# Performance work log

Measured on AMD Instinct MI355X. Metric: run time of the kernel, lower is better.

## Reference

```python
import jax, jax.numpy as jnp
import numpy as np


def setup_inputs() -> dict:
    key = jax.random.key(0)
    k1, k2, k3, k4 = jax.random.split(key, 4)
    B, T, S, D = 256, 16, 32, 768
    return {
        "video_global": jax.random.normal(k1, (B, D), dtype=jnp.float32),
        "text_global": jax.random.normal(k2, (B, D), dtype=jnp.float32),
        "video_local": jax.random.normal(k3, (B, T, D), dtype=jnp.float32),
        "text_local": jax.random.normal(k4, (B, S, D), dtype=jnp.float32),
        "temp": jnp.zeros((1,), dtype=jnp.float32),  # log(1.0)
    }


def reference(video_global, text_global, video_local, text_local, temp):
    B = video_global.shape[0]
    logit_scale = jnp.exp(temp)[0]

    # ---- global contrastive loss ----
    global_sim = logit_scale * (video_global @ text_global.T)  # [B, B]
    diag = jnp.arange(B)
    loss_v2t = -jax.nn.log_softmax(global_sim, axis=1)[diag, diag].mean()
    loss_t2v = -jax.nn.log_softmax(global_sim, axis=0)[diag, diag].mean()
    loss_global = 0.5 * (loss_v2t + loss_t2v)

    # ---- local positive scores ----
    # paired (diagonal) local similarity: [B, T, S]
    sim_pos = logit_scale * jnp.einsum("btd,bsd->bts", video_local, text_local)
    time_weights = jax.nn.softmax(sim_pos.max(axis=-1), axis=-1)  # [B, T]
    pos_scores = (sim_pos.mean(axis=-1) * time_weights).sum(axis=1)  # [B]

    # ---- local negative scores (batched pairwise contraction) ----
    # [B, B, T, S]: video i vs text j, replacing the B*(B-1) tiny einsum loop
    sim_all = logit_scale * jnp.einsum("btd,csd->bcts", video_local, text_local)
    neg_full = (time_weights[:, None, :] * sim_all.mean(axis=-1)).sum(axis=-1)  # [B, B]

    # drop diagonal (i == j), preserving row-major loop order
    rows, cols = np.nonzero(~np.eye(B, dtype=bool))
    neg_scores = neg_full[rows, cols].reshape(B, B - 1)

    logits = jnp.concatenate([pos_scores[:, None], neg_scores], axis=-1)  # [B, B]
    loss_local = -jax.nn.log_softmax(logits, axis=-1)[:, 0].mean()

    return 0.6 * loss_global + 0.4 * loss_local
```

## Files before the change

### kernel.cpp

```cpp
#include <hip/hip_runtime.h>
#include <cmath>

#define BB 256
#define TT 16
#define SS 32
#define DD 768
#define LROW 260

__global__ __launch_bounds__(512) void hl_stage1(
    const float* __restrict__ vl, const float* __restrict__ tl,
    const float* __restrict__ temp,
    float* __restrict__ vw_ws, float* __restrict__ tb_ws)
{
    __shared__ float smem[12480];
    __shared__ float simb[512];
    __shared__ float rmax[16];
    __shared__ float twb[16];

    const int i   = blockIdx.x;
    const int tid = threadIdx.x;
    const float lsc = expf(temp[0]);

    const int slice = tid & 15;
    const int g     = tid >> 4;
    const int tg    = g >> 3;
    const int sg    = g & 7;

    const float* vli = vl + (size_t)i * TT * DD;
    const float* tli = tl + (size_t)i * SS * DD;

    float acc[4][4];
#pragma unroll
    for (int a = 0; a < 4; ++a)
#pragma unroll
        for (int b = 0; b < 4; ++b) acc[a][b] = 0.f;

    for (int c = 0; c < 3; ++c) {
        const int d0 = c << 8;
#pragma unroll
        for (int k = 0; k < 2; ++k) {
            int f4 = tid + (k << 9);
            int r  = f4 >> 6;
            int dc = (f4 & 63) << 2;
            *(float4*)&smem[r * LROW + dc] = *(const float4*)&vli[r * DD + d0 + dc];
        }
#pragma unroll
        for (int k = 0; k < 4; ++k) {
            int f4 = tid + (k << 9);
            int r  = f4 >> 6;
            int dc = (f4 & 63) << 2;
            *(float4*)&smem[(16 + r) * LROW + dc] = *(const float4*)&tli[r * DD + d0 + dc];
        }
        __syncthreads();
#pragma unroll
        for (int step = 0; step < 4; ++step) {
            const int db = (slice << 4) + (step << 2);
            float4 av[4], bv[4];
#pragma unroll
            for (int ti = 0; ti < 4; ++ti)
                av[ti] = *(const float4*)&smem[(tg * 4 + ti) * LROW + db];
#pragma unroll
            for (int sj = 0; sj < 4; ++sj)
                bv[sj] = *(const float4*)&smem[(16 + sg * 4 + sj) * LROW + db];
#pragma unroll
            for (int ti = 0; ti < 4; ++ti)
#pragma unroll
                for (int sj = 0; sj < 4; ++sj)
                    acc[ti][sj] += av[ti].x * bv[sj].x + av[ti].y * bv[sj].y
                                 + av[ti].z * bv[sj].z + av[ti].w * bv[sj].w;
        }
        __syncthreads();
    }

#pragma unroll
    for (int ti = 0; ti < 4; ++ti)
#pragma unroll
        for (int sj = 0; sj < 4; ++sj) {
            int t = tg * 4 + ti, s = sg * 4 + sj;
            smem[(t * 32 + s) * 17 + slice] = acc[ti][sj];
        }
    __syncthreads();
    {
        float ssum = 0.f;
#pragma unroll
        for (int k = 0; k < 16; ++k) ssum += smem[tid * 17 + k];
        simb[tid] = lsc * ssum;
    }
    __syncthreads();
    if (tid < 16) {
        float m = -3.0e38f;
        for (int s = 0; s < 32; ++s)
            m = fmaxf(m, simb[tid * 32 + ((s + tid) & 31)]);
        rmax[tid] = m;
    }
    __syncthreads();
    if (tid == 0) {
        float M = -3.0e38f;
        for (int t = 0; t < 16; ++t) M = fmaxf(M, rmax[t]);
        float ssum = 0.f;
        for (int t = 0; t < 16; ++t) {
            float e = expf(rmax[t] - M);
            twb[t] = e;
            ssum += e;
        }
        float inv = 1.0f / ssum;
        for (int t = 0; t < 16; ++t) twb[t] *= inv;
    }
    __syncthreads();

    for (int d = tid; d < DD; d += 512) {
        float vwv = 0.f;
#pragma unroll
        for (int t = 0; t < 16; ++t) vwv += twb[t] * vli[t * DD + d];
        vw_ws[(size_t)i * DD + d] = vwv;
        float tbv = 0.f;
#pragma unroll
        for (int s = 0; s < 32; ++s) tbv += tli[s * DD + d];
        tb_ws[(size_t)i * DD + d] = tbv * (1.0f / 32.0f);
    }
}

__global__ __launch_bounds__(256) void hl_gemm(
    const float* __restrict__ vg, const float* __restrict__ tg,
    const float* __restrict__ vw, const float* __restrict__ tb,
    const float* __restrict__ temp, float* __restrict__ cparts)
{
    __shared__ float As[16][68];
    __shared__ float Bs[16][68];
    __shared__ float Tb[64][68];

    const int b   = blockIdx.x;
    const int p   = b & 7;
    const int tj  = (b >> 3) & 3;
    const int ti  = (b >> 5) & 3;
    const int mat = b >> 7;
    const int tid = threadIdx.x;
    const float lsc = expf(temp[0]);

    const float* A  = mat ? vw : vg;
    const float* Bm = mat ? tb : tg;
    const int i0 = ti * 64, j0 = tj * 64, kb0 = p * 96;

    const int srow = tid >> 2, skq = tid & 3;
    const int tr = tid >> 4, tc = tid & 15;

    float acc[4][4];
#pragma unroll
    for (int r = 0; r < 4; ++r)
#pragma unroll
        for (int cc = 0; cc < 4; ++cc) acc[r][cc] = 0.f;

    for (int ch = 0; ch < 6; ++ch) {
        const int kb = kb0 + ch * 16;
        float4 a4 = *(const float4*)&A [(size_t)(i0 + srow) * DD + kb + skq * 4];
        float4 b4 = *(const float4*)&Bm[(size_t)(j0 + srow) * DD + kb + skq * 4];
        __syncthreads();
        As[skq * 4 + 0][srow] = a4.x; As[skq * 4 + 1][srow] = a4.y;
        As[skq * 4 + 2][srow] = a4.z; As[skq * 4 + 3][srow] = a4.w;
        Bs[skq * 4 + 0][srow] = b4.x; Bs[skq * 4 + 1][srow] = b4.y;
        Bs[skq * 4 + 2][srow] = b4.z; Bs[skq * 4 + 3][srow] = b4.w;
        __syncthreads();
#pragma unroll
        for (int k = 0; k < 16; ++k) {
            float4 av = *(const float4*)&As[k][tr * 4];
            float4 bv = *(const float4*)&Bs[k][tc * 4];
            float ar[4] = {av.x, av.y, av.z, av.w};
            float br[4] = {bv.x, bv.y, bv.z, bv.w};
#pragma unroll
            for (int r = 0; r < 4; ++r)
#pragma unroll
                for (int cc = 0; cc < 4; ++cc)
                    acc[r][cc] += ar[r] * br[cc];
        }
    }

    const int cm = mat ? 0 : 1;
    float* Cp = cparts + ((size_t)p * 3 + cm) * 65536;
#pragma unroll
    for (int r = 0; r < 4; ++r) {
        float4 v = {acc[r][0] * lsc, acc[r][1] * lsc, acc[r][2] * lsc, acc[r][3] * lsc};
        *(float4*)&Cp[(size_t)(i0 + tr * 4 + r) * 256 + j0 + tc * 4] = v;
    }
    if (mat == 0) {
        __syncthreads();
#pragma unroll
        for (int r = 0; r < 4; ++r)
#pragma unroll
            for (int cc = 0; cc < 4; ++cc)
                Tb[tc * 4 + cc][tr * 4 + r] = acc[r][cc] * lsc;
        __syncthreads();
        float* Ct = cparts + ((size_t)p * 3 + 2) * 65536;
#pragma unroll
        for (int r = 0; r < 4; ++r) {
            float4 v = *(const float4*)&Tb[tr * 4 + r][tc * 4];
            *(float4*)&Ct[(size_t)(j0 + tr * 4 + r) * 256 + i0 + tc * 4] = v;
        }
    }
}

__global__ __launch_bounds__(256) void hl_lse(
    const float* __restrict__ cparts, float* __restrict__ out)
{
    __shared__ float xs[256];
    __shared__ float wred[4];
    __shared__ float bcast;

    const int b   = blockIdx.x;
    const int cm  = b >> 8;
    const int row = b & 255;
    const int tid = threadIdx.x;

    float x = 0.f;
#pragma unroll
    for (int p = 0; p < 8; ++p)
        x += cparts[((size_t)p * 3 + cm) * 65536 + (size_t)row * 256 + tid];
    xs[tid] = x;

    float m = x;
#pragma unroll
    for (int off = 32; off > 0; off >>= 1)
        m = fmaxf(m, __shfl_down(m, off, 64));
    if ((tid & 63) == 0) wred[tid >> 6] = m;
    __syncthreads();
    if (tid == 0)
        bcast = fmaxf(fmaxf(wred[0], wred[1]), fmaxf(wred[2], wred[3]));
    __syncthreads();
    float M = bcast;
    float e = expf(x - M);
#pragma unroll
    for (int off = 32; off > 0; off >>= 1)
        e += __shfl_down(e, off, 64);
    if ((tid & 63) == 0) wred[tid >> 6] = e;
    __syncthreads();
    if (tid == 0) {
        float Stot = wred[0] + wred[1] + wred[2] + wred[3];
        float lse  = M + logf(Stot);
        float w    = (cm == 0) ? (0.4f / 256.0f) : (0.3f / 256.0f);
        atomicAdd(out, w * (lse - xs[row]));
    }
}

extern "C" void kernel_launch(void* const* d_in, const int* in_sizes, int n_in,
                              void* d_out, int out_size, void* d_ws, size_t ws_size,
                              hipStream_t stream)
{
    const float* vg   = (const float*)d_in[0];
    const float* tg   = (const float*)d_in[1];
    const float* vl   = (const float*)d_in[2];
    const float* tl   = (const float*)d_in[3];
    const float* temp = (const float*)d_in[4];
    float* out = (float*)d_out;

    float* vw     = (float*)d_ws;
    float* tb     = vw + (size_t)BB * DD;
    float* cparts = tb + (size_t)BB * DD;

    hipMemsetAsync(out, 0, sizeof(float) * out_size, stream);
    hl_stage1<<<dim3(BB),  dim3(512), 0, stream>>>(vl, tl, temp, vw, tb);
    hl_gemm  <<<dim3(256), dim3(256), 0, stream>>>(vg, tg, vw, tb, temp, cparts);
    hl_lse   <<<dim3(768), dim3(256), 0, stream>>>(cparts, out);
}
```

Before: 118.0 us.

## Prefetch next chunk into registers, compute text mean from LDS, drop memset

Stage1 now loads the next 256-wide d-chunk of video/text local rows into registers while the current chunk is being multiplied, giving a register double-buffer over global loads. The text-mean reduction is computed from the already-staged LDS tile instead of re-reading text_local from global memory at the end. The LDS access pattern for the dot products is changed to interleave slices, which should reduce bank conflicts. The output zeroing moves into the first kernel, removing the separate memset launch at the cost of more register pressure in stage1.

```diff
diff --git a/kernel.cpp b/kernel.cpp
--- a/kernel.cpp
+++ b/kernel.cpp
@@ -2,15 +2,14 @@
 #include <cmath>
 
 #define BB 256
-#define TT 16
-#define SS 32
 #define DD 768
 #define LROW 260
 
 __global__ __launch_bounds__(512) void hl_stage1(
     const float* __restrict__ vl, const float* __restrict__ tl,
     const float* __restrict__ temp,
-    float* __restrict__ vw_ws, float* __restrict__ tb_ws)
+    float* __restrict__ vw_ws, float* __restrict__ tb_ws,
+    float* __restrict__ out)
 {
     __shared__ float smem[12480];
     __shared__ float simb[512];
@@ -19,6 +18,7 @@
 
     const int i   = blockIdx.x;
     const int tid = threadIdx.x;
+    if (i == 0 && tid == 0) out[0] = 0.f;
     const float lsc = expf(temp[0]);
 
     const int slice = tid & 15;
@@ -26,8 +26,20 @@
     const int tg    = g >> 3;
     const int sg    = g & 7;
 
-    const float* vli = vl + (size_t)i * TT * DD;
-    const float* tli = tl + (size_t)i * SS * DD;
+    const float* vli = vl + (size_t)i * 16 * DD;
+    const float* tli = tl + (size_t)i * 32 * DD;
+
+    float4 va[2], ta[4];
+#pragma unroll
+    for (int k = 0; k < 2; ++k) {
+        int f4 = tid + (k << 9);
+        va[k] = *(const float4*)&vli[(f4 >> 6) * DD + ((f4 & 63) << 2)];
+    }
+#pragma unroll
+    for (int k = 0; k < 4; ++k) {
+        int f4 = tid + (k << 9);
+        ta[k] = *(const float4*)&tli[(f4 >> 6) * DD + ((f4 & 63) << 2)];
+    }
 
     float acc[4][4];
 #pragma unroll
@@ -36,25 +48,33 @@
         for (int b = 0; b < 4; ++b) acc[a][b] = 0.f;
 
     for (int c = 0; c < 3; ++c) {
-        const int d0 = c << 8;
 #pragma unroll
         for (int k = 0; k < 2; ++k) {
             int f4 = tid + (k << 9);
-            int r  = f4 >> 6;
-            int dc = (f4 & 63) << 2;
-            *(float4*)&smem[r * LROW + dc] = *(const float4*)&vli[r * DD + d0 + dc];
+            *(float4*)&smem[(f4 >> 6) * LROW + ((f4 & 63) << 2)] = va[k];
         }
 #pragma unroll
         for (int k = 0; k < 4; ++k) {
             int f4 = tid + (k << 9);
-            int r  = f4 >> 6;
-            int dc = (f4 & 63) << 2;
-            *(float4*)&smem[(16 + r) * LROW + dc] = *(const float4*)&tli[r * DD + d0 + dc];
-        }
-        __syncthreads();
+            *(float4*)&smem[(16 + (f4 >> 6)) * LROW + ((f4 & 63) << 2)] = ta[k];
+        }
+        __syncthreads();
+        if (c < 2) {
+            const int d0 = (c + 1) << 8;
+#pragma unroll
+            for (int k = 0; k < 2; ++k) {
+                int f4 = tid + (k << 9);
+                va[k] = *(const float4*)&vli[(f4 >> 6) * DD + d0 + ((f4 & 63) << 2)];
+            }
+#pragma unroll
+            for (int k = 0; k < 4; ++k) {
+                int f4 = tid + (k << 9);
+                ta[k] = *(const float4*)&tli[(f4 >> 6) * DD + d0 + ((f4 & 63) << 2)];
+            }
+        }
 #pragma unroll
         for (int step = 0; step < 4; ++step) {
-            const int db = (slice << 4) + (step << 2);
+            const int db = (step << 6) + (slice << 2);
             float4 av[4], bv[4];
 #pragma unroll
             for (int ti = 0; ti < 4; ++ti)
@@ -68,6 +88,12 @@
                 for (int sj = 0; sj < 4; ++sj)
                     acc[ti][sj] += av[ti].x * bv[sj].x + av[ti].y * bv[sj].y
                                  + av[ti].z * bv[sj].z + av[ti].w * bv[sj].w;
+        }
+        if (tid < 256) {
+            float s2 = 0.f;
+#pragma unroll
+            for (int s = 0; s < 32; ++s) s2 += smem[(16 + s) * LROW + tid];
+            tb_ws[(size_t)i * DD + (c << 8) + tid] = s2 * (1.0f / 32.0f);
         }
         __syncthreads();
     }
@@ -113,10 +139,6 @@
 #pragma unroll
         for (int t = 0; t < 16; ++t) vwv += twb[t] * vli[t * DD + d];
         vw_ws[(size_t)i * DD + d] = vwv;
-        float tbv = 0.f;
-#pragma unroll
-        for (int s = 0; s < 32; ++s) tbv += tli[s * DD + d];
-        tb_ws[(size_t)i * DD + d] = tbv * (1.0f / 32.0f);
     }
 }
 
@@ -255,8 +277,7 @@
     float* tb     = vw + (size_t)BB * DD;
     float* cparts = tb + (size_t)BB * DD;
 
-    hipMemsetAsync(out, 0, sizeof(float) * out_size, stream);
-    hl_stage1<<<dim3(BB),  dim3(512), 0, stream>>>(vl, tl, temp, vw, tb);
+    hl_stage1<<<dim3(BB),  dim3(512), 0, stream>>>(vl, tl, temp, vw, tb, out);
     hl_gemm  <<<dim3(256), dim3(256), 0, stream>>>(vg, tg, vw, tb, temp, cparts);
     hl_lse   <<<dim3(768), dim3(256), 0, stream>>>(cparts, out);
 }
```

Result: slower. 123.9 us (+5.0%).
